# Kernel optimization log

Measured on AMD Instinct MI355X. Metric: run time of the kernel, lower is better.

Reference implementation:

```python
import jax, jax.numpy as jnp
import numpy as np

B, S, D, H = 4, 1024, 1024, 16
HD = D // H  # head dim = 64


def setup_inputs() -> dict:
    key = jax.random.key(0)
    ks = jax.random.split(key, 7)
    return {
        "x": jax.random.normal(ks[0], (B, S, D), dtype=jnp.float32),
        "w_attn": jax.random.normal(ks[1], (D, 3 * D), dtype=jnp.float32) * 0.02,
        "b_attn": jax.random.normal(ks[2], (3 * D,), dtype=jnp.float32) * 0.02,
        "w_proj": jax.random.normal(ks[3], (D, D), dtype=jnp.float32) * 0.02,
        "b_proj": jax.random.normal(ks[4], (D,), dtype=jnp.float32) * 0.02,
        "attn_override": jax.random.uniform(ks[5], (H, S, S), dtype=jnp.float32),
        "attn_override_mask": jax.random.randint(ks[6], (H, S, S), 0, 2).astype(bool),
    }


def reference(x, w_attn, b_attn, w_proj, b_proj, attn_override, attn_override_mask):
    # c_attn (GPT-2 Conv1D): x @ W + b, then split into q, k, v
    qkv = jnp.einsum("bsd,de->bse", x, w_attn) + b_attn
    q, k, v = jnp.split(qkv, 3, axis=-1)
    # split heads: q,v -> [B,H,S,hd]; k -> [B,H,hd,S]
    q = q.reshape(B, S, H, HD).transpose(0, 2, 1, 3)
    k = k.reshape(B, S, H, HD).transpose(0, 2, 3, 1)
    v = v.reshape(B, S, H, HD).transpose(0, 2, 1, 3)
    # present buffer: stack(key.transpose(-2,-1), value) -> [2,B,H,S,hd]
    present = jnp.stack((k.transpose(0, 1, 3, 2), v))
    # scores with scaling
    w = jnp.einsum("bhqd,bhdk->bhqk", q, k) / jnp.sqrt(jnp.asarray(HD, x.dtype))
    # GPT-2 causal bias: w*b - 10000*(1-b)
    b = jnp.tril(jnp.ones((S, S), dtype=x.dtype))[None, None]
    w = w * b - 10000.0 * (1.0 - b)
    w = jax.nn.softmax(w, axis=-1)
    # attn_dropout: identity (eval). Override attention weights (broadcast over batch).
    w = jnp.where(attn_override_mask[None], attn_override[None], w)
    a = jnp.einsum("bhqk,bhkd->bhqd", w, v)
    # merge heads -> [B,S,D], then c_proj; resid_dropout identity (eval)
    a = a.transpose(0, 2, 1, 3).reshape(B, S, D)
    a = jnp.einsum("bsd,de->bse", a, w_proj) + b_proj
    return a, present
```

## Files before the change

### kernel.cpp

```cpp
#include <hip/hip_runtime.h>
#include <hip/hip_bf16.h>

#define Bdim 4
#define Sdim 1024
#define Ddim 1024
#define Hdim 16
#define HDdim 64

typedef __attribute__((ext_vector_type(8))) short short8;
typedef __attribute__((ext_vector_type(4))) float f32x4;
typedef __attribute__((ext_vector_type(2))) unsigned int uint2v;

#define AS1 __attribute__((address_space(1)))
#define AS3 __attribute__((address_space(3)))

__device__ __forceinline__ unsigned short f2bf(float x) {
    unsigned int u = __builtin_bit_cast(unsigned int, x);
    return (unsigned short)((u + 0x7fffu + ((u >> 16) & 1u)) >> 16);
}

__global__ __launch_bounds__(256) void conv_bf16(const float* __restrict__ in,
                                                 unsigned short* __restrict__ out) {
    int i = blockIdx.x * 256 + threadIdx.x;
    float4 v = ((const float4*)in)[i];
    uint2v p;
    p.x = (unsigned)f2bf(v.x) | ((unsigned)f2bf(v.y) << 16);
    p.y = (unsigned)f2bf(v.z) | ((unsigned)f2bf(v.w) << 16);
    ((uint2v*)out)[i] = p;
}

__global__ __launch_bounds__(256) void transpose_bf16(const float* __restrict__ W,
                                                      unsigned short* __restrict__ Wt,
                                                      int K, int N) {
    __shared__ float t[32][33];
    const int tk = blockIdx.y * 32, tn = blockIdx.x * 32;
    const int r = threadIdx.x >> 5, c = threadIdx.x & 31;
    #pragma unroll
    for (int j = 0; j < 4; j++)
        t[r + 8 * j][c] = W[(size_t)(tk + r + 8 * j) * N + tn + c];
    __syncthreads();
    #pragma unroll
    for (int j = 0; j < 4; j++) {
        int nn = r + 8 * j;
        Wt[(size_t)(tn + nn) * K + tk + c] = f2bf(t[c][nn]);
    }
}

#define GEMM_BODY(Aptr, Bptr)                                                          \
    __shared__ unsigned short As[128 * 32];                                            \
    __shared__ unsigned short Bs[128 * 32];                                            \
    const int tid = threadIdx.x;                                                       \
    const int lane = tid & 63, w = tid >> 6;                                           \
    const int wm = w >> 1, wn = w & 1;                                                 \
    const int l15 = lane & 15, lg = lane >> 4;                                         \
    const int tile_m = blockIdx.y * 128, tile_n = blockIdx.x * 128;                    \
    f32x4 acc[4][4] = {};                                                              \
    for (int k0 = 0; k0 < 1024; k0 += 32) {                                            \
        _Pragma("unroll")                                                              \
        for (int j = 0; j < 2; j++) {                                                  \
            int ca = j * 256 + tid;                                                    \
            int rowa = ca >> 2, offa = (ca & 3) * 16;                                  \
            const char* ga = (const char*)(Aptr) +                                     \
                ((size_t)(tile_m + rowa) * 1024 + k0) * 2 + offa;                      \
            char* la = (char*)As + (j * 256 + w * 64) * 16;                            \
            __builtin_amdgcn_global_load_lds((const AS1 void*)ga, (AS3 void*)la,       \
                                             16, 0, 0);                                \
            const char* gb = (const char*)(Bptr) +                                     \
                ((size_t)(tile_n + rowa) * 1024 + k0) * 2 + offa;                      \
            char* lb = (char*)Bs + (j * 256 + w * 64) * 16;                            \
            __builtin_amdgcn_global_load_lds((const AS1 void*)gb, (AS3 void*)lb,       \
                                             16, 0, 0);                                \
        }                                                                              \
        __syncthreads();                                                               \
        short8 af[4], bfr[4];                                                          \
        _Pragma("unroll")                                                              \
        for (int t4 = 0; t4 < 4; t4++) {                                               \
            af[t4] = *(const short8*)((const char*)As +                                \
                        (wm * 64 + t4 * 16 + l15) * 64 + lg * 16);                     \
            bfr[t4] = *(const short8*)((const char*)Bs +                               \
                        (wn * 64 + t4 * 16 + l15) * 64 + lg * 16);                     \
        }                                                                              \
        _Pragma("unroll")                                                              \
        for (int i = 0; i < 4; i++)                                                    \
            _Pragma("unroll")                                                          \
            for (int j2 = 0; j2 < 4; j2++)                                             \
                acc[i][j2] = __builtin_amdgcn_mfma_f32_16x16x32_bf16(                  \
                    af[i], bfr[j2], acc[i][j2], 0, 0, 0);                              \
        __syncthreads();                                                               \
    }

__global__ __launch_bounds__(256) void gemm_qkv_mfma(const unsigned short* __restrict__ Xb,
                                                     const unsigned short* __restrict__ Wt,
                                                     const float* __restrict__ bias,
                                                     unsigned short* __restrict__ qbuf,
                                                     float* __restrict__ kout,
                                                     float* __restrict__ vout) {
    GEMM_BODY(Xb, Wt)
    const int seg = tile_n >> 10;
    #pragma unroll
    for (int i = 0; i < 4; i++) {
        #pragma unroll
        for (int j2 = 0; j2 < 4; j2++) {
            int n = tile_n + wn * 64 + j2 * 16 + l15;
            float bv = bias[n];
            int nn = n & 1023, h = nn >> 6, d = nn & 63;
            #pragma unroll
            for (int r = 0; r < 4; r++) {
                int m = tile_m + wm * 64 + i * 16 + 4 * lg + r;
                float v = acc[i][j2][r] + bv;
                int bb = m >> 10, s = m & 1023;
                size_t oidx = ((size_t)((bb * Hdim + h) * Sdim + s)) * HDdim + d;
                if (seg == 0) qbuf[oidx] = f2bf(v * 0.125f);
                else if (seg == 1) kout[oidx] = v;
                else vout[oidx] = v;
            }
        }
    }
}

__global__ __launch_bounds__(256) void gemm_proj_mfma(const unsigned short* __restrict__ Ab,
                                                      const unsigned short* __restrict__ Wt,
                                                      const float* __restrict__ bias,
                                                      float* __restrict__ out) {
    GEMM_BODY(Ab, Wt)
    #pragma unroll
    for (int i = 0; i < 4; i++) {
        #pragma unroll
        for (int j2 = 0; j2 < 4; j2++) {
            int n = tile_n + wn * 64 + j2 * 16 + l15;
            float bv = bias[n];
            #pragma unroll
            for (int r = 0; r < 4; r++) {
                int m = tile_m + wm * 64 + i * 16 + 4 * lg + r;
                out[(size_t)m * Ddim + n] = acc[i][j2][r] + bv;
            }
        }
    }
}

__global__ __launch_bounds__(256) void attn_mfma(const unsigned short* __restrict__ qbuf,
                                                 const float* __restrict__ kbuf,
                                                 const float* __restrict__ vbuf,
                                                 const float* __restrict__ ovr,
                                                 const int* __restrict__ msk,
                                                 unsigned short* __restrict__ abuf) {
    const int qt = blockIdx.x;
    const int bh = blockIdx.y;
    const int h = bh & (Hdim - 1);
    const int b = bh >> 4;
    const int tid = threadIdx.x;
    const int wq = tid >> 6;
    const int lane = tid & 63;
    const int l15 = lane & 15;
    const int lg = lane >> 4;

    __shared__ unsigned short Ks[64 * 64];
    __shared__ unsigned short Vt[64 * 64];
    __shared__ unsigned short Ps[4][16 * 64];

    const float* kb = kbuf + (size_t)bh * Sdim * HDdim;
    const float* vb = vbuf + (size_t)bh * Sdim * HDdim;
    const int qrow = qt * 64 + wq * 16 + l15;

    short8 qf[2];
    {
        const unsigned short* qr = qbuf + ((size_t)bh * Sdim + qrow) * HDdim;
        qf[0] = *(const short8*)(qr + 8 * lg);
        qf[1] = *(const short8*)(qr + 8 * lg + 32);
    }

    auto stageK = [&](int kt) {
        #pragma unroll
        for (int j = 0; j < 4; j++) {
            int idx = tid + j * 256;
            int k = idx >> 4;
            int d0 = (idx & 15) * 4;
            float4 v = *(const float4*)(kb + (size_t)(kt * 64 + k) * HDdim + d0);
            uint2v p;
            p.x = (unsigned)f2bf(v.x) | ((unsigned)f2bf(v.y) << 16);
            p.y = (unsigned)f2bf(v.z) | ((unsigned)f2bf(v.w) << 16);
            int byte = k * 128 + d0 * 2;
            byte ^= (k & 7) << 4;
            *(uint2v*)((char*)Ks + byte) = p;
        }
    };
    auto stageV = [&](int kt) {
        int d = tid & 63;
        int k00 = 4 * (tid >> 6);
        #pragma unroll
        for (int j = 0; j < 4; j++) {
            int k0 = k00 + 16 * j;
            float v0 = vb[(size_t)(kt * 64 + k0 + 0) * HDdim + d];
            float v1 = vb[(size_t)(kt * 64 + k0 + 1) * HDdim + d];
            float v2 = vb[(size_t)(kt * 64 + k0 + 2) * HDdim + d];
            float v3 = vb[(size_t)(kt * 64 + k0 + 3) * HDdim + d];
            uint2v p;
            p.x = (unsigned)f2bf(v0) | ((unsigned)f2bf(v1) << 16);
            p.y = (unsigned)f2bf(v2) | ((unsigned)f2bf(v3) << 16);
            int byte = d * 128 + k0 * 2;
            byte ^= (d & 7) << 4;
            *(uint2v*)((char*)Vt + byte) = p;
        }
    };
    auto readfrag = [&](const unsigned short* base, int row, int f) -> short8 {
        int byte = row * 128 + lg * 16 + f * 64;
        byte ^= (row & 7) << 4;
        return *(const short8*)((const char*)base + byte);
    };

    float m_run = -1e30f, l_run = 0.f;
    for (int kt = 0; kt <= qt; kt++) {
        __syncthreads();
        stageK(kt);
        __syncthreads();
        float sv[16];
        const bool diag = (kt == qt);
        #pragma unroll
        for (int ks = 0; ks < 4; ks++) {
            f32x4 c = {0.f, 0.f, 0.f, 0.f};
            short8 a0 = readfrag(Ks, l15 + 16 * ks, 0);
            short8 a1 = readfrag(Ks, l15 + 16 * ks, 1);
            c = __builtin_amdgcn_mfma_f32_16x16x32_bf16(a0, qf[0], c, 0, 0, 0);
            c = __builtin_amdgcn_mfma_f32_16x16x32_bf16(a1, qf[1], c, 0, 0, 0);
            #pragma unroll
            for (int r = 0; r < 4; r++) {
                int kg = kt * 64 + ks * 16 + 4 * lg + r;
                float s = c[r];
                if (diag && kg > qrow) s = -1e30f;
                sv[ks * 4 + r] = s;
            }
        }
        float tm = -1e30f;
        #pragma unroll
        for (int i = 0; i < 16; i++) tm = fmaxf(tm, sv[i]);
        tm = fmaxf(tm, __shfl_xor(tm, 16));
        tm = fmaxf(tm, __shfl_xor(tm, 32));
        float mn = fmaxf(m_run, tm);
        float ts = 0.f;
        #pragma unroll
        for (int i = 0; i < 16; i++) ts += __expf(sv[i] - mn);
        ts += __shfl_xor(ts, 16);
        ts += __shfl_xor(ts, 32);
        l_run = l_run * __expf(m_run - mn) + ts;
        m_run = mn;
    }
    const float inv_l = 1.f / l_run;

    f32x4 acc[4];
    #pragma unroll
    for (int ds = 0; ds < 4; ds++) acc[ds] = (f32x4){0.f, 0.f, 0.f, 0.f};
    const float* ob_base = ovr + ((size_t)h * Sdim + qrow) * Sdim;
    const int* mb_base = msk + ((size_t)h * Sdim + qrow) * Sdim;

    for (int kt = 0; kt < 16; kt++) {
        __syncthreads();
        if (kt <= qt) stageK(kt);
        stageV(kt);
        __syncthreads();

        float w[16];
        if (kt <= qt) {
            const bool diag = (kt == qt);
            #pragma unroll
            for (int ks = 0; ks < 4; ks++) {
                f32x4 c = {0.f, 0.f, 0.f, 0.f};
                short8 a0 = readfrag(Ks, l15 + 16 * ks, 0);
                short8 a1 = readfrag(Ks, l15 + 16 * ks, 1);
                c = __builtin_amdgcn_mfma_f32_16x16x32_bf16(a0, qf[0], c, 0, 0, 0);
                c = __builtin_amdgcn_mfma_f32_16x16x32_bf16(a1, qf[1], c, 0, 0, 0);
                #pragma unroll
                for (int r = 0; r < 4; r++) {
                    int kg = kt * 64 + ks * 16 + 4 * lg + r;
                    float p = __expf(c[r] - m_run) * inv_l;
                    if (diag && kg > qrow) p = 0.f;
                    w[ks * 4 + r] = p;
                }
            }
        } else {
            #pragma unroll
            for (int i = 0; i < 16; i++) w[i] = 0.f;
        }
        #pragma unroll
        for (int ks = 0; ks < 4; ks++) {
            int kb0 = kt * 64 + ks * 16 + 4 * lg;
            float4 o4 = *(const float4*)(ob_base + kb0);
            int4 m4 = *(const int4*)(mb_base + kb0);
            if (m4.x) w[ks * 4 + 0] = o4.x;
            if (m4.y) w[ks * 4 + 1] = o4.y;
            if (m4.z) w[ks * 4 + 2] = o4.z;
            if (m4.w) w[ks * 4 + 3] = o4.w;
        }
        #pragma unroll
        for (int ks = 0; ks < 4; ks++) {
            #pragma unroll
            for (int r = 0; r < 4; r++) {
                int kloc = ks * 16 + 4 * lg + r;
                int byte = l15 * 128 + kloc * 2;
                byte ^= (l15 & 7) << 4;
                *(unsigned short*)((char*)(Ps[wq]) + byte) = f2bf(w[ks * 4 + r]);
            }
        }
        short8 pa0 = readfrag(Ps[wq], l15, 0);
        short8 pa1 = readfrag(Ps[wq], l15, 1);
        #pragma unroll
        for (int ds = 0; ds < 4; ds++) {
            short8 v0 = readfrag(Vt, l15 + 16 * ds, 0);
            short8 v1 = readfrag(Vt, l15 + 16 * ds, 1);
            acc[ds] = __builtin_amdgcn_mfma_f32_16x16x32_bf16(pa0, v0, acc[ds], 0, 0, 0);
            acc[ds] = __builtin_amdgcn_mfma_f32_16x16x32_bf16(pa1, v1, acc[ds], 0, 0, 0);
        }
    }

    #pragma unroll
    for (int ds = 0; ds < 4; ds++) {
        #pragma unroll
        for (int r = 0; r < 4; r++) {
            int q = qt * 64 + wq * 16 + 4 * lg + r;
            int d = h * HDdim + ds * 16 + l15;
            abuf[((size_t)(b * Sdim + q)) * Ddim + d] = f2bf(acc[ds][r]);
        }
    }
}

extern "C" void kernel_launch(void* const* d_in, const int* in_sizes, int n_in,
                              void* d_out, int out_size, void* d_ws, size_t ws_size,
                              hipStream_t stream) {
    const float* x       = (const float*)d_in[0];
    const float* w_attn  = (const float*)d_in[1];
    const float* b_attn  = (const float*)d_in[2];
    const float* w_proj  = (const float*)d_in[3];
    const float* b_proj  = (const float*)d_in[4];
    const float* ovr     = (const float*)d_in[5];
    const int*   msk     = (const int*)d_in[6];

    float* out = (float*)d_out;
    float* a_out = out;
    float* kout  = out + (size_t)Bdim * Sdim * Ddim;
    float* vout  = kout + (size_t)Bdim * Hdim * Sdim * HDdim;

    char* ws = (char*)d_ws;
    unsigned short* qbuf = (unsigned short*)ws;
    unsigned short* abuf = (unsigned short*)(ws + (8  << 20));
    unsigned short* Xb   = (unsigned short*)(ws + (16 << 20));
    unsigned short* Wta  = (unsigned short*)(ws + (24 << 20));
    unsigned short* Wtp  = (unsigned short*)(ws + (30 << 20));

    conv_bf16<<<dim3(4096), 256, 0, stream>>>(x, Xb);
    transpose_bf16<<<dim3(96, 32), 256, 0, stream>>>(w_attn, Wta, 1024, 3072);
    transpose_bf16<<<dim3(32, 32), 256, 0, stream>>>(w_proj, Wtp, 1024, 1024);

    gemm_qkv_mfma<<<dim3(24, 32), 256, 0, stream>>>(Xb, Wta, b_attn, qbuf, kout, vout);

    attn_mfma<<<dim3(16, 64), 256, 0, stream>>>(qbuf, kout, vout, ovr, msk, abuf);

    gemm_proj_mfma<<<dim3(8, 32), 256, 0, stream>>>(abuf, Wtp, b_proj, a_out);
}
```

Before: 413.8 us.

## Precompact override/mask and pre-transpose bf16 K/V to drop LDS staging in attention

Adds a prep kernel that converts the fp32 attention override to bf16 and packs the int mask into 64-bit ballot bitmasks. A second prep kernel converts K to bf16 and writes V transposed in bf16. The attention kernel then reads K and V fragments straight from global memory, with no LDS staging and no block-wide barriers, and reads the compact override and mask bits. This cuts the repeated per-batch traffic on the large override and mask tensors. The cost is two extra launches, extra workspace, and uncoalesced-ish direct global fragment loads that rely on cache hits.

```diff
diff --git a/kernel.cpp b/kernel.cpp
--- a/kernel.cpp
+++ b/kernel.cpp
@@ -10,6 +10,7 @@
 typedef __attribute__((ext_vector_type(8))) short short8;
 typedef __attribute__((ext_vector_type(4))) float f32x4;
 typedef __attribute__((ext_vector_type(2))) unsigned int uint2v;
+typedef __attribute__((ext_vector_type(4))) unsigned short ushort4v;
 
 #define AS1 __attribute__((address_space(1)))
 #define AS3 __attribute__((address_space(3)))
@@ -17,6 +18,10 @@
 __device__ __forceinline__ unsigned short f2bf(float x) {
     unsigned int u = __builtin_bit_cast(unsigned int, x);
     return (unsigned short)((u + 0x7fffu + ((u >> 16) & 1u)) >> 16);
+}
+__device__ __forceinline__ float bf2f(unsigned short u) {
+    unsigned int v = ((unsigned int)u) << 16;
+    return __builtin_bit_cast(float, v);
 }
 
 __global__ __launch_bounds__(256) void conv_bf16(const float* __restrict__ in,
@@ -43,6 +48,51 @@
     for (int j = 0; j < 4; j++) {
         int nn = r + 8 * j;
         Wt[(size_t)(tn + nn) * K + tk + c] = f2bf(t[c][nn]);
+    }
+}
+
+__global__ __launch_bounds__(256) void ovr_prep(const float* __restrict__ ovr,
+                                                const int* __restrict__ msk,
+                                                unsigned short* __restrict__ ovrb,
+                                                unsigned long long* __restrict__ mbits) {
+    size_t i = (size_t)blockIdx.x * 256 + threadIdx.x;
+    ovrb[i] = f2bf(ovr[i]);
+    unsigned long long bal = __ballot(msk[i] != 0);
+    if ((threadIdx.x & 63) == 0) mbits[i >> 6] = bal;
+}
+
+__global__ __launch_bounds__(256) void kv_prep(const float* __restrict__ kout,
+                                               const float* __restrict__ vout,
+                                               unsigned short* __restrict__ Kb,
+                                               unsigned short* __restrict__ Vtr) {
+    const int bh = blockIdx.y;
+    const int s0 = blockIdx.x * 64;
+    const int tid = threadIdx.x;
+    __shared__ float t[64][65];
+    const float4* kbase = (const float4*)(kout + ((size_t)bh * Sdim + s0) * HDdim);
+    const float4* vbase = (const float4*)(vout + ((size_t)bh * Sdim + s0) * HDdim);
+    uint2v* kb = (uint2v*)(Kb + ((size_t)bh * Sdim + s0) * HDdim);
+    #pragma unroll
+    for (int i = 0; i < 4; i++) {
+        int idx = tid + i * 256;
+        float4 v = kbase[idx];
+        uint2v p;
+        p.x = (unsigned)f2bf(v.x) | ((unsigned)f2bf(v.y) << 16);
+        p.y = (unsigned)f2bf(v.z) | ((unsigned)f2bf(v.w) << 16);
+        kb[idx] = p;
+        float4 vv = vbase[idx];
+        int r = idx >> 4, c = (idx & 15) * 4;
+        t[r][c + 0] = vv.x; t[r][c + 1] = vv.y; t[r][c + 2] = vv.z; t[r][c + 3] = vv.w;
+    }
+    __syncthreads();
+    #pragma unroll
+    for (int i = 0; i < 4; i++) {
+        int idx = tid + i * 256;
+        int d = idx >> 4, sc = (idx & 15) * 4;
+        uint2v p;
+        p.x = (unsigned)f2bf(t[sc + 0][d]) | ((unsigned)f2bf(t[sc + 1][d]) << 16);
+        p.y = (unsigned)f2bf(t[sc + 2][d]) | ((unsigned)f2bf(t[sc + 3][d]) << 16);
+        *(uint2v*)(Vtr + (size_t)bh * HDdim * Sdim + (size_t)d * Sdim + s0 + sc) = p;
     }
 }
 
@@ -138,12 +188,12 @@
     }
 }
 
-__global__ __launch_bounds__(256) void attn_mfma(const unsigned short* __restrict__ qbuf,
-                                                 const float* __restrict__ kbuf,
-                                                 const float* __restrict__ vbuf,
-                                                 const float* __restrict__ ovr,
-                                                 const int* __restrict__ msk,
-                                                 unsigned short* __restrict__ abuf) {
+__global__ __launch_bounds__(256) void attn_mfma2(const unsigned short* __restrict__ qbuf,
+                                                  const unsigned short* __restrict__ Kb,
+                                                  const unsigned short* __restrict__ Vtr,
+                                                  const unsigned short* __restrict__ ovrb,
+                                                  const unsigned long long* __restrict__ mbits,
+                                                  unsigned short* __restrict__ abuf) {
     const int qt = blockIdx.x;
     const int bh = blockIdx.y;
     const int h = bh & (Hdim - 1);
@@ -154,12 +204,10 @@
     const int l15 = lane & 15;
     const int lg = lane >> 4;
 
-    __shared__ unsigned short Ks[64 * 64];
-    __shared__ unsigned short Vt[64 * 64];
     __shared__ unsigned short Ps[4][16 * 64];
 
-    const float* kb = kbuf + (size_t)bh * Sdim * HDdim;
-    const float* vb = vbuf + (size_t)bh * Sdim * HDdim;
+    const unsigned short* kb = Kb + (size_t)bh * Sdim * HDdim;
+    const unsigned short* vt = Vtr + (size_t)bh * HDdim * Sdim;
     const int qrow = qt * 64 + wq * 16 + l15;
 
     short8 qf[2];
@@ -169,57 +217,16 @@
         qf[1] = *(const short8*)(qr + 8 * lg + 32);
     }
 
-    auto stageK = [&](int kt) {
-        #pragma unroll
-        for (int j = 0; j < 4; j++) {
-            int idx = tid + j * 256;
-            int k = idx >> 4;
-            int d0 = (idx & 15) * 4;
-            float4 v = *(const float4*)(kb + (size_t)(kt * 64 + k) * HDdim + d0);
-            uint2v p;
-            p.x = (unsigned)f2bf(v.x) | ((unsigned)f2bf(v.y) << 16);
-            p.y = (unsigned)f2bf(v.z) | ((unsigned)f2bf(v.w) << 16);
-            int byte = k * 128 + d0 * 2;
-            byte ^= (k & 7) << 4;
-            *(uint2v*)((char*)Ks + byte) = p;
-        }
-    };
-    auto stageV = [&](int kt) {
-        int d = tid & 63;
-        int k00 = 4 * (tid >> 6);
-        #pragma unroll
-        for (int j = 0; j < 4; j++) {
-            int k0 = k00 + 16 * j;
-            float v0 = vb[(size_t)(kt * 64 + k0 + 0) * HDdim + d];
-            float v1 = vb[(size_t)(kt * 64 + k0 + 1) * HDdim + d];
-            float v2 = vb[(size_t)(kt * 64 + k0 + 2) * HDdim + d];
-            float v3 = vb[(size_t)(kt * 64 + k0 + 3) * HDdim + d];
-            uint2v p;
-            p.x = (unsigned)f2bf(v0) | ((unsigned)f2bf(v1) << 16);
-            p.y = (unsigned)f2bf(v2) | ((unsigned)f2bf(v3) << 16);
-            int byte = d * 128 + k0 * 2;
-            byte ^= (d & 7) << 4;
-            *(uint2v*)((char*)Vt + byte) = p;
-        }
-    };
-    auto readfrag = [&](const unsigned short* base, int row, int f) -> short8 {
-        int byte = row * 128 + lg * 16 + f * 64;
-        byte ^= (row & 7) << 4;
-        return *(const short8*)((const char*)base + byte);
-    };
-
     float m_run = -1e30f, l_run = 0.f;
     for (int kt = 0; kt <= qt; kt++) {
-        __syncthreads();
-        stageK(kt);
-        __syncthreads();
         float sv[16];
         const bool diag = (kt == qt);
         #pragma unroll
         for (int ks = 0; ks < 4; ks++) {
+            const unsigned short* krow = kb + (size_t)(kt * 64 + ks * 16 + l15) * HDdim;
+            short8 a0 = *(const short8*)(krow + 8 * lg);
+            short8 a1 = *(const short8*)(krow + 8 * lg + 32);
             f32x4 c = {0.f, 0.f, 0.f, 0.f};
-            short8 a0 = readfrag(Ks, l15 + 16 * ks, 0);
-            short8 a1 = readfrag(Ks, l15 + 16 * ks, 1);
             c = __builtin_amdgcn_mfma_f32_16x16x32_bf16(a0, qf[0], c, 0, 0, 0);
             c = __builtin_amdgcn_mfma_f32_16x16x32_bf16(a1, qf[1], c, 0, 0, 0);
             #pragma unroll
@@ -249,23 +256,19 @@
     f32x4 acc[4];
     #pragma unroll
     for (int ds = 0; ds < 4; ds++) acc[ds] = (f32x4){0.f, 0.f, 0.f, 0.f};
-    const float* ob_base = ovr + ((size_t)h * Sdim + qrow) * Sdim;
-    const int* mb_base = msk + ((size_t)h * Sdim + qrow) * Sdim;
+    const unsigned short* ob_base = ovrb + ((size_t)h * Sdim + qrow) * Sdim;
+    const unsigned long long* mb_base = mbits + ((size_t)h * Sdim + qrow) * (Sdim / 64);
 
     for (int kt = 0; kt < 16; kt++) {
-        __syncthreads();
-        if (kt <= qt) stageK(kt);
-        stageV(kt);
-        __syncthreads();
-
         float w[16];
         if (kt <= qt) {
             const bool diag = (kt == qt);
             #pragma unroll
             for (int ks = 0; ks < 4; ks++) {
+                const unsigned short* krow = kb + (size_t)(kt * 64 + ks * 16 + l15) * HDdim;
+                short8 a0 = *(const short8*)(krow + 8 * lg);
+                short8 a1 = *(const short8*)(krow + 8 * lg + 32);
                 f32x4 c = {0.f, 0.f, 0.f, 0.f};
-                short8 a0 = readfrag(Ks, l15 + 16 * ks, 0);
-                short8 a1 = readfrag(Ks, l15 + 16 * ks, 1);
                 c = __builtin_amdgcn_mfma_f32_16x16x32_bf16(a0, qf[0], c, 0, 0, 0);
                 c = __builtin_amdgcn_mfma_f32_16x16x32_bf16(a1, qf[1], c, 0, 0, 0);
                 #pragma unroll
@@ -280,32 +283,34 @@
             #pragma unroll
             for (int i = 0; i < 16; i++) w[i] = 0.f;
         }
+        unsigned long long mw = mb_base[kt];
         #pragma unroll
         for (int ks = 0; ks < 4; ks++) {
             int kb0 = kt * 64 + ks * 16 + 4 * lg;
-            float4 o4 = *(const float4*)(ob_base + kb0);
-            int4 m4 = *(const int4*)(mb_base + kb0);
-            if (m4.x) w[ks * 4 + 0] = o4.x;
-            if (m4.y) w[ks * 4 + 1] = o4.y;
-            if (m4.z) w[ks * 4 + 2] = o4.z;
-            if (m4.w) w[ks * 4 + 3] = o4.w;
+            ushort4v o4 = *(const ushort4v*)(ob_base + kb0);
+            int bit0 = ks * 16 + 4 * lg;
+            #pragma unroll
+            for (int r = 0; r < 4; r++)
+                if ((mw >> (bit0 + r)) & 1ULL) w[ks * 4 + r] = bf2f(o4[r]);
         }
         #pragma unroll
         for (int ks = 0; ks < 4; ks++) {
-            #pragma unroll
-            for (int r = 0; r < 4; r++) {
-                int kloc = ks * 16 + 4 * lg + r;
-                int byte = l15 * 128 + kloc * 2;
-                byte ^= (l15 & 7) << 4;
-                *(unsigned short*)((char*)(Ps[wq]) + byte) = f2bf(w[ks * 4 + r]);
-            }
-        }
-        short8 pa0 = readfrag(Ps[wq], l15, 0);
-        short8 pa1 = readfrag(Ps[wq], l15, 1);
+            uint2v p;
+            p.x = (unsigned)f2bf(w[ks * 4 + 0]) | ((unsigned)f2bf(w[ks * 4 + 1]) << 16);
+            p.y = (unsigned)f2bf(w[ks * 4 + 2]) | ((unsigned)f2bf(w[ks * 4 + 3]) << 16);
+            int byte = l15 * 128 + (ks * 16 + 4 * lg) * 2;
+            byte ^= (l15 & 7) << 4;
+            *(uint2v*)((char*)(Ps[wq]) + byte) = p;
+        }
+        int pbyte0 = l15 * 128 + lg * 16;
+        pbyte0 ^= (l15 & 7) << 4;
+        short8 pa0 = *(const short8*)((const char*)(Ps[wq]) + pbyte0);
+        short8 pa1 = *(const short8*)((const char*)(Ps[wq]) + (pbyte0 ^ 64));
         #pragma unroll
         for (int ds = 0; ds < 4; ds++) {
-            short8 v0 = readfrag(Vt, l15 + 16 * ds, 0);
-            short8 v1 = readfrag(Vt, l15 + 16 * ds, 1);
+            const unsigned short* vrow = vt + (size_t)(ds * 16 + l15) * Sdim + kt * 64;
+            short8 v0 = *(const short8*)(vrow + 8 * lg);
+            short8 v1 = *(const short8*)(vrow + 8 * lg + 32);
             acc[ds] = __builtin_amdgcn_mfma_f32_16x16x32_bf16(pa0, v0, acc[ds], 0, 0, 0);
             acc[ds] = __builtin_amdgcn_mfma_f32_16x16x32_bf16(pa1, v1, acc[ds], 0, 0, 0);
         }
@@ -344,14 +349,21 @@
     unsigned short* Xb   = (unsigned short*)(ws + (16 << 20));
     unsigned short* Wta  = (unsigned short*)(ws + (24 << 20));
     unsigned short* Wtp  = (unsigned short*)(ws + (30 << 20));
+    unsigned short* Kb   = (unsigned short*)(ws + (32 << 20));
+    unsigned short* Vtr  = (unsigned short*)(ws + (40 << 20));
+    unsigned short* ovrb = (unsigned short*)(ws + (48 << 20));
+    unsigned long long* mbits = (unsigned long long*)(ws + (80 << 20));
 
     conv_bf16<<<dim3(4096), 256, 0, stream>>>(x, Xb);
     transpose_bf16<<<dim3(96, 32), 256, 0, stream>>>(w_attn, Wta, 1024, 3072);
     transpose_bf16<<<dim3(32, 32), 256, 0, stream>>>(w_proj, Wtp, 1024, 1024);
+    ovr_prep<<<dim3(65536), 256, 0, stream>>>(ovr, msk, ovrb, mbits);
 
     gemm_qkv_mfma<<<dim3(24, 32), 256, 0, stream>>>(Xb, Wta, b_attn, qbuf, kout, vout);
 
-    attn_mfma<<<dim3(16, 64), 256, 0, stream>>>(qbuf, kout, vout, ovr, msk, abuf);
+    kv_prep<<<dim3(16, 64), 256, 0, stream>>>(kout, vout, Kb, Vtr);
+
+    attn_mfma2<<<dim3(16, 64), 256, 0, stream>>>(qbuf, Kb, Vtr, ovrb, mbits, abuf);
 
     gemm_proj_mfma<<<dim3(8, 32), 256, 0, stream>>>(abuf, Wtp, b_proj, a_out);
 }
```

Measured after the change: 471.8 us. 14.0% more time.
